# Kernel tuning notes

Measured on AMD Instinct MI355X. Metric: run time of the kernel, lower is better.

## Reference

```python
import jax, jax.numpy as jnp
import numpy as np

EPS = 1e-06

def setup_inputs() -> dict:
    key = jax.random.key(0)
    kx, kq, kk, kv = jax.random.split(key, 4)
    B, S, D, F = 8, 4096, 1024, 1024
    # glorot-uniform-ish scale for weights
    scale = (6.0 / (D + F)) ** 0.5
    x = jax.random.normal(kx, (B, S, D), dtype=jnp.float32)
    Wq = jax.random.uniform(kq, (D, F), dtype=jnp.float32, minval=-scale, maxval=scale)
    Wk = jax.random.uniform(kk, (D, F), dtype=jnp.float32, minval=-scale, maxval=scale)
    Wv = jax.random.uniform(kv, (D, F), dtype=jnp.float32, minval=-scale, maxval=scale)
    return {"x": x, "Wq": Wq, "Wk": Wk, "Wv": Wv}


def reference(x, Wq, Wk, Wv):
    # x: [B, S, D]; projections -> [B, S, F]
    queries = jnp.einsum('bsd,df->bsf', x, Wq)
    keys = jnp.einsum('bsd,df->bsf', x, Wk)
    values = jnp.einsum('bsd,df->bsf', x, Wv)
    # feature map: relu(.) + 1 (strictly positive kernel features)
    queries = jax.nn.relu(queries) + 1.0
    keys = jax.nn.relu(keys) + 1.0
    # numerator: K^T V over sequence -> [B, F, F]
    numerator = jnp.einsum('bsf,bsg->bfg', keys, values)
    # denominator: sum of keys over sequence -> [B, 1, F]; broadcasts over last axis
    denominator = jnp.sum(keys, axis=-2, keepdims=True)
    context = numerator / (denominator + EPS)
    # output: context @ Q^T -> [B, F, S]
    output = jnp.einsum('bfg,bsg->bfs', context, queries)
    return output
```

## Files before the change

### kernel.cpp

```cpp
#include <hip/hip_runtime.h>


#define EPSF 1e-6f

constexpr int Bb = 8;
constexpr int Ss = 4096;
constexpr int Dd = 1024;
constexpr int Ff = 1024;

typedef __attribute__((ext_vector_type(8))) short   bf16x8;
typedef __attribute__((ext_vector_type(8))) unsigned short u16x8;
typedef __attribute__((ext_vector_type(4))) float   f32x4;

typedef __attribute__((address_space(3))) unsigned char lds_u8;
typedef __attribute__((address_space(3))) const bf16x8  lds_cvec;

static __device__ __forceinline__ unsigned short f2bf(float f) {
    union { float f; unsigned int u; } v; v.f = f;
    unsigned int r = (v.u + 0x7fffu + ((v.u >> 16) & 1u)) >> 16;
    return (unsigned short)r;
}
static __device__ __forceinline__ float bf2f(unsigned short u) {
    union { unsigned int u; float f; } v; v.u = ((unsigned int)u) << 16;
    return v.f;
}

static __device__ __forceinline__ void gld_lds16(const void* g, lds_u8* l) {
    __builtin_amdgcn_global_load_lds(
        (const __attribute__((address_space(1))) unsigned int*)g,
        (__attribute__((address_space(3))) unsigned int*)l,
        16, 0, 0);
}

__global__ void cvt_x_kernel(const float* __restrict__ x, unsigned short* __restrict__ xb, int n4)
{
    int i = blockIdx.x * blockDim.x + threadIdx.x;
    if (i >= n4) return;
    float4 v = *(const float4*)&x[(size_t)i * 4];
    ushort4 o;
    o.x = f2bf(v.x); o.y = f2bf(v.y); o.z = f2bf(v.z); o.w = f2bf(v.w);
    *(ushort4*)&xb[(size_t)i * 4] = o;
}

__global__ void cvt_wT_kernel(const float* __restrict__ Wq,
                              const float* __restrict__ Wk,
                              const float* __restrict__ Wv,
                              unsigned short* __restrict__ WT)
{
    const int z = blockIdx.z;
    const float* __restrict__ W = (z == 0) ? Wq : (z == 1 ? Wk : Wv);
    unsigned short* __restrict__ dst = WT + (size_t)z * Dd * Ff;

    __shared__ float tile[32][33];
    const int tid = threadIdx.x;
    const int d0 = blockIdx.y * 32, f0 = blockIdx.x * 32;
    const int c = tid & 31, r8 = tid >> 5;
#pragma unroll
    for (int p = 0; p < 4; ++p) {
        int r = p * 8 + r8;
        tile[r][c] = W[(size_t)(d0 + r) * Ff + f0 + c];
    }
    __syncthreads();
#pragma unroll
    for (int p = 0; p < 4; ++p) {
        int r = p * 8 + r8;
        dst[(size_t)(f0 + r) * Dd + d0 + c] = f2bf(tile[c][r]);
    }
}

__global__ void add_ctx_kernel(const unsigned short* __restrict__ p,
                               unsigned short* __restrict__ c)
{
    const int b = blockIdx.y;
    const size_t i8 = ((size_t)blockIdx.x * 256 + threadIdx.x) * 8;
    const u16x8 a0 = *(const u16x8*)(p + (size_t)(2 * b) * Ff * Ff + i8);
    const u16x8 a1 = *(const u16x8*)(p + (size_t)(2 * b + 1) * Ff * Ff + i8);
    u16x8 o;
#pragma unroll
    for (int j = 0; j < 8; ++j) o[j] = f2bf(bf2f(a0[j]) + bf2f(a1[j]));
    *(u16x8*)(c + (size_t)b * Ff * Ff + i8) = o;
}

template<int ACT, int SCALE, int OUT_BF16, int SPLITK2, int DENACC, int KVSEL>
__global__ __launch_bounds__(512, 2)
void gemm8(const unsigned short* __restrict__ A,
           const unsigned short* __restrict__ Bt,
           void* __restrict__ Cout,
           const float* __restrict__ den,
           float* __restrict__ denw,
           int lda, int ldb, int ldc, int Kdim,
           size_t strideA, size_t strideB, size_t strideC)
{
    __shared__ __align__(16) unsigned char smem_[131072];
    lds_u8* const smem = (lds_u8*)smem_;

    const int gx = gridDim.x, gxy = gx * gridDim.y;
    int flat = blockIdx.z * gxy + blockIdx.y * gx + blockIdx.x;
    const int nwg = gxy * gridDim.z;
    const int cpx = nwg >> 3;
    flat = (flat & 7) * cpx + (flat >> 3);
    const int z = flat / gxy;
    const int rem = flat - z * gxy;
    const int by = rem / gx;
    const int bx = rem - by * gx;

    const int pid  = KVSEL ? (z & 1) : 0;
    const int zb   = KVSEL ? (z >> 1) : (SPLITK2 ? (z >> 1) : z);
    const int koff = SPLITK2 ? ((z & 1) * Kdim) : 0;
    const size_t cslab = KVSEL ? (size_t)(pid * Bb + zb) : (size_t)z;

    const unsigned short* __restrict__ Ag  =
        A + strideA * zb + koff + (KVSEL ? (size_t)pid * Dd * Ff : 0);
    const unsigned short* __restrict__ Bg  = Bt + strideB * zb + koff;
    const float* __restrict__ denb = SCALE ? (den + (size_t)zb * Ff) : nullptr;

    const int bm = by * 256;
    const int bn = bx * 256;

    const int tid  = threadIdx.x;
    const int wv   = tid >> 6, lane = tid & 63;
    const int wm   = wv >> 2, wn = wv & 3;
    const int lm   = lane & 15;
    const int kg16 = (lane >> 4) << 4;
    const int swz  = (lm & 7) << 4;
    const int kbs  = (((tid & 7) ^ ((tid >> 3) & 7)) << 4);
    const int srow = tid >> 3;

    f32x4 acc[8][4];
#pragma unroll
    for (int i = 0; i < 8; ++i)
#pragma unroll
        for (int j = 0; j < 4; ++j) acc[i][j] = (f32x4){0.f, 0.f, 0.f, 0.f};

    lds_u8* const A0 = smem;
    lds_u8* const B0 = smem + 32768;
    lds_u8* const A1 = smem + 65536;
    lds_u8* const B1 = smem + 98304;

    auto STAGE = [&](int ts, int m, int buf, int h) {
        const unsigned short* gb = m ? Bg : Ag;
        const int ld = m ? ldb : lda;
        const int off0 = m ? bn : bm;
        lds_u8* lb = smem + buf * 65536 + m * 32768 + h * 16384 + wv * 1024;
#pragma unroll
        for (int q = 0; q < 2; ++q) {
            int row = h * 128 + q * 64 + srow;
            const unsigned char* g =
                (const unsigned char*)(gb + (size_t)(off0 + row) * ld + ts * 64) + kbs;
            gld_lds16(g, lb + q * 8192);
        }
    };
    auto LDA4 = [&](bf16x8* dst, int fmb, int kk, lds_u8* Ab) {
#pragma unroll
        for (int f = 0; f < 4; ++f) {
            int r = wm * 128 + (fmb + f) * 16 + lm;
            dst[f] = *(lds_cvec*)(Ab + r * 128 + ((kk * 64 + kg16) ^ swz));
        }
    };
    auto LDB4 = [&](bf16x8* dst, int kk, lds_u8* Bb) {
#pragma unroll
        for (int f = 0; f < 4; ++f) {
            int c = wn * 64 + f * 16 + lm;
            dst[f] = *(lds_cvec*)(Bb + c * 128 + ((kk * 64 + kg16) ^ swz));
        }
    };

#define MM16(a4, b4, mo)                                                        \
    do {                                                                        \
        __builtin_amdgcn_s_setprio(1);                                          \
        _Pragma("unroll")                                                       \
        for (int fm = 0; fm < 4; ++fm)                                          \
            _Pragma("unroll")                                                   \
            for (int fn = 0; fn < 4; ++fn)                                      \
                acc[(mo) + fm][fn] = __builtin_amdgcn_mfma_f32_16x16x32_bf16(   \
                    (b4)[fn], (a4)[fm], acc[(mo) + fm][fn], 0, 0, 0);           \
        __builtin_amdgcn_s_setprio(0);                                          \
    } while (0)

#define PHEND()                                                     \
    do {                                                            \
        asm volatile("s_waitcnt lgkmcnt(0)");                       \
        __builtin_amdgcn_sched_barrier(0);                          \
        __builtin_amdgcn_s_barrier();                               \
    } while (0)
#define PHEND_VM2()                                                 \
    do {                                                            \
        asm volatile("s_waitcnt vmcnt(2) lgkmcnt(0)");              \
        __builtin_amdgcn_sched_barrier(0);                          \
        __builtin_amdgcn_s_barrier();                               \
    } while (0)

    const int NT = Kdim >> 6;
    const int NI = NT >> 1;

    STAGE(0, 1, 0, 0); STAGE(0, 1, 0, 1);
    STAGE(0, 0, 0, 0); STAGE(0, 0, 0, 1);
    STAGE(1, 1, 1, 0); STAGE(1, 1, 1, 1);
    asm volatile("s_waitcnt vmcnt(4)");
    __builtin_amdgcn_s_barrier();

    bf16x8 a03[4], a47[4], b0[4], b1[4];
    LDB4(b0, 0, B0); LDA4(a03, 0, 0, A0);

    for (int i = 0; i < NI; ++i) {
        const int t = 2 * i;
        const int t1s = t + 1;
        const int t2s = (t + 2 < NT) ? t + 2 : NT - 1;
        const int t3s = (t + 3 < NT) ? t + 3 : NT - 1;

        STAGE(t1s, 0, 1, 0);
        LDA4(a47, 4, 0, A0);
        MM16(a03, b0, 0);
        PHEND();
        STAGE(t1s, 0, 1, 1);
        LDA4(a03, 0, 1, A0); LDB4(b1, 1, B0);
        MM16(a47, b0, 4);
        PHEND();
        STAGE(t2s, 1, 0, 0);
        LDA4(a47, 4, 1, A0);
        MM16(a03, b1, 0);
        PHEND_VM2();
        STAGE(t2s, 1, 0, 1);
        LDA4(a03, 0, 0, A1); LDB4(b0, 0, B1);
        MM16(a47, b1, 4);
        PHEND();
        STAGE(t2s, 0, 0, 0);
        LDA4(a47, 4, 0, A1);
        MM16(a03, b0, 0);
        PHEND();
        STAGE(t2s, 0, 0, 1);
        LDA4(a03, 0, 1, A1); LDB4(b1, 1, B1);
        MM16(a47, b0, 4);
        PHEND();
        STAGE(t3s, 1, 1, 0);
        LDA4(a47, 4, 1, A1);
        MM16(a03, b1, 0);
        PHEND_VM2();
        STAGE(t3s, 1, 1, 1);
        LDA4(a03, 0, 0, A0); LDB4(b0, 0, B0);
        MM16(a47, b1, 4);
        PHEND();
    }

    asm volatile("s_waitcnt vmcnt(0)");

    const bool actv = ACT || (KVSEL && pid == 0);
    const bool dacc = DENACC || (KVSEL && pid == 0);
    const int hi4 = (lane >> 4) * 4;
#pragma unroll
    for (int fm = 0; fm < 8; ++fm) {
        const int gr = bm + wm * 128 + fm * 16 + lm;
        float rowsum = 0.f;
#pragma unroll
        for (int fn = 0; fn < 4; ++fn) {
            const int gcn = bn + wn * 64 + fn * 16 + hi4;
            f32x4 v = acc[fm][fn];
            if (actv) {
#pragma unroll
                for (int e = 0; e < 4; ++e) v[e] = fmaxf(v[e], 0.f) + 1.f;
            }
            if (dacc) rowsum += v[0] + v[1] + v[2] + v[3];
            if (SCALE) {
                float4 d4 = *(const float4*)&denb[gcn];
                v[0] *= 1.f / (d4.x + EPSF);
                v[1] *= 1.f / (d4.y + EPSF);
                v[2] *= 1.f / (d4.z + EPSF);
                v[3] *= 1.f / (d4.w + EPSF);
            }
            if (OUT_BF16) {
                ushort4 o;
                o.x = f2bf(v[0]); o.y = f2bf(v[1]); o.z = f2bf(v[2]); o.w = f2bf(v[3]);
                *(ushort4*)((unsigned short*)Cout + strideC * cslab + (size_t)gr * ldc + gcn) = o;
            } else {
                *(float4*)((float*)Cout + strideC * cslab + (size_t)gr * ldc + gcn) =
                    *(float4*)&v;
            }
        }
        if (dacc) {
            rowsum += __shfl_xor(rowsum, 16, 64);
            rowsum += __shfl_xor(rowsum, 32, 64);
            if (lane < 16) atomicAdd(denw + (size_t)zb * Ff + gr, rowsum);
        }
    }
#undef MM16
#undef PHEND
#undef PHEND_VM2
}

extern "C" void kernel_launch(void* const* d_in, const int* in_sizes, int n_in,
                              void* d_out, int out_size, void* d_ws, size_t ws_size,
                              hipStream_t stream)
{
    (void)in_sizes; (void)n_in; (void)out_size;
    const float* x  = (const float*)d_in[0];
    const float* Wq = (const float*)d_in[1];
    const float* Wk = (const float*)d_in[2];
    const float* Wv = (const float*)d_in[3];
    float* out = (float*)d_out;

    const size_t nx   = (size_t)Bb * Ss * Dd;
    const size_t nW   = (size_t)3 * Dd * Ff;
    const size_t nQKV = (size_t)Bb * Ss * Ff;
    const size_t nCtx = (size_t)Bb * Ff * Ff;
    const size_t nP   = (size_t)16 * Ff * Ff;

    unsigned short* xb   = (unsigned short*)d_ws;
    unsigned short* WT   = xb + nx;
    unsigned short* Qb   = WT + nW;
    unsigned short* KbT  = Qb + nQKV;
    unsigned short* VbT  = KbT + nQKV;
    unsigned short* ctxb = VbT + nQKV;
    float* den = (float*)(ctxb + nCtx);
    unsigned short* pctx = (unsigned short*)(den + (size_t)Bb * Ff);

    const size_t need_split =
        ((nx + nW + 3 * nQKV + nCtx + nP) * 2 + (size_t)Bb * Ff * 4);
    const bool do_split = ws_size >= need_split;

    cvt_x_kernel<<<dim3((int)(nx / 4 / 256)), 256, 0, stream>>>(x, xb, (int)(nx / 4));
    cvt_wT_kernel<<<dim3(Ff / 32, Dd / 32, 3), 256, 0, stream>>>(Wq, Wk, Wv, WT);

    hipMemsetAsync(den, 0, (size_t)Bb * Ff * sizeof(float), stream);

    gemm8<0, 0, 1, 0, 0, 1><<<dim3(Ss / 256, Ff / 256, 2 * Bb), 512, 0, stream>>>(
        WT + (size_t)1 * Dd * Ff, xb, KbT, nullptr, den,
        Dd, Dd, Ss, Dd, 0, (size_t)Ss * Dd, (size_t)Ff * Ss);

    gemm8<1, 1, 1, 0, 0, 0><<<dim3(Ff / 256, Ss / 256, Bb), 512, 0, stream>>>(
        xb, WT + (size_t)0 * Dd * Ff, Qb, den, nullptr,
        Dd, Dd, Ff, Dd, (size_t)Ss * Dd, 0, (size_t)Ss * Ff);

    if (do_split) {
        gemm8<0, 0, 1, 1, 0, 0><<<dim3(Ff / 256, Ff / 256, 2 * Bb), 512, 0, stream>>>(
            KbT, VbT, pctx, nullptr, nullptr,
            Ss, Ss, Ff, Ss / 2, (size_t)Ff * Ss, (size_t)Ff * Ss, (size_t)Ff * Ff);
        add_ctx_kernel<<<dim3(Ff * Ff / 8 / 256, Bb), 256, 0, stream>>>(pctx, ctxb);
    } else {
        gemm8<0, 0, 1, 0, 0, 0><<<dim3(Ff / 256, Ff / 256, Bb), 512, 0, stream>>>(
            KbT, VbT, ctxb, nullptr, nullptr,
            Ss, Ss, Ff, Ss, (size_t)Ff * Ss, (size_t)Ff * Ss, (size_t)Ff * Ff);
    }

    gemm8<0, 0, 0, 0, 0, 0><<<dim3(Ss / 256, Ff / 256, Bb), 512, 0, stream>>>(
        ctxb, Qb, out, nullptr, nullptr,
        Ff, Ff, Ss, Ff, (size_t)Ff * Ff, (size_t)Ss * Ff, (size_t)Ff * Ss);
}
```

Baseline: 407.5 us.

## Fuse Q, K, V projections into one launch and move denominator scaling to context

The Q projection GEMM and the combined K/V projection GEMM are merged into a single launch with 3*B slabs, where the slab index picks the projection and its output layout. Before, Q had to wait for the K denominator, so it was scaled by 1/den inside its epilogue. That scaling now happens on the context matrix, in the split-K add kernel or in the non-split context GEMM epilogue, which removes the dependency between the two launches. The intent is fewer launches, a better-filled grid, and less tail imbalance. The risks are an uneven mix of tile orientations inside one grid and the extra den loads in the add kernel.

```diff
diff --git a/kernel.cpp b/kernel.cpp
--- a/kernel.cpp
+++ b/kernel.cpp
@@ -69,19 +69,25 @@
 }
 
 __global__ void add_ctx_kernel(const unsigned short* __restrict__ p,
-                               unsigned short* __restrict__ c)
+                               unsigned short* __restrict__ c,
+                               const float* __restrict__ den)
 {
     const int b = blockIdx.y;
     const size_t i8 = ((size_t)blockIdx.x * 256 + threadIdx.x) * 8;
+    const int g0 = (int)(i8 & (size_t)(Ff - 1));
     const u16x8 a0 = *(const u16x8*)(p + (size_t)(2 * b) * Ff * Ff + i8);
     const u16x8 a1 = *(const u16x8*)(p + (size_t)(2 * b + 1) * Ff * Ff + i8);
+    const float4 d0 = *(const float4*)&den[(size_t)b * Ff + g0];
+    const float4 d1 = *(const float4*)&den[(size_t)b * Ff + g0 + 4];
+    const float dv[8] = {d0.x, d0.y, d0.z, d0.w, d1.x, d1.y, d1.z, d1.w};
     u16x8 o;
 #pragma unroll
-    for (int j = 0; j < 8; ++j) o[j] = f2bf(bf2f(a0[j]) + bf2f(a1[j]));
+    for (int j = 0; j < 8; ++j)
+        o[j] = f2bf((bf2f(a0[j]) + bf2f(a1[j])) * (1.f / (dv[j] + EPSF)));
     *(u16x8*)(c + (size_t)b * Ff * Ff + i8) = o;
 }
 
-template<int ACT, int SCALE, int OUT_BF16, int SPLITK2, int DENACC, int KVSEL>
+template<int ACT, int SCALE, int OUT_BF16, int SPLITK2, int DENACC, int QKV>
 __global__ __launch_bounds__(512, 2)
 void gemm8(const unsigned short* __restrict__ A,
            const unsigned short* __restrict__ Bt,
@@ -104,18 +110,40 @@
     const int by = rem / gx;
     const int bx = rem - by * gx;
 
-    const int pid  = KVSEL ? (z & 1) : 0;
-    const int zb   = KVSEL ? (z >> 1) : (SPLITK2 ? (z >> 1) : z);
+    const int pid  = QKV ? (z % 3) : 0;
+    const int zb   = QKV ? (z / 3) : (SPLITK2 ? (z >> 1) : z);
     const int koff = SPLITK2 ? ((z & 1) * Kdim) : 0;
-    const size_t cslab = KVSEL ? (size_t)(pid * Bb + zb) : (size_t)z;
-
-    const unsigned short* __restrict__ Ag  =
-        A + strideA * zb + koff + (KVSEL ? (size_t)pid * Dd * Ff : 0);
-    const unsigned short* __restrict__ Bg  = Bt + strideB * zb + koff;
+
+    const unsigned short* __restrict__ Ag;
+    const unsigned short* __restrict__ Bg;
+    int bm, bn, ldcr;
+    size_t coff;
+    bool actv, dacc;
+    if (QKV) {
+        if (pid == 0) {
+            Ag = Bt + (size_t)zb * Ss * Dd;
+            Bg = A;
+            bm = bx * 256; bn = by * 256;
+            ldcr = Ff;
+            coff = (size_t)zb * Ss * Ff;
+            actv = true;  dacc = false;
+        } else {
+            Ag = A + (size_t)pid * Dd * Ff;
+            Bg = Bt + (size_t)zb * Ss * Dd;
+            bm = by * 256; bn = bx * 256;
+            ldcr = Ss;
+            coff = ((size_t)pid * Bb + zb) * ((size_t)Ff * Ss);
+            actv = (pid == 1); dacc = (pid == 1);
+        }
+    } else {
+        Ag = A + strideA * zb + koff;
+        Bg = Bt + strideB * zb + koff;
+        bm = by * 256; bn = bx * 256;
+        ldcr = ldc;
+        coff = strideC * (size_t)z;
+        actv = ACT; dacc = DENACC;
+    }
     const float* __restrict__ denb = SCALE ? (den + (size_t)zb * Ff) : nullptr;
-
-    const int bm = by * 256;
-    const int bn = bx * 256;
 
     const int tid  = threadIdx.x;
     const int wv   = tid >> 6, lane = tid & 63;
@@ -244,8 +272,6 @@
 
     asm volatile("s_waitcnt vmcnt(0)");
 
-    const bool actv = ACT || (KVSEL && pid == 0);
-    const bool dacc = DENACC || (KVSEL && pid == 0);
     const int hi4 = (lane >> 4) * 4;
 #pragma unroll
     for (int fm = 0; fm < 8; ++fm) {
@@ -270,9 +296,9 @@
             if (OUT_BF16) {
                 ushort4 o;
                 o.x = f2bf(v[0]); o.y = f2bf(v[1]); o.z = f2bf(v[2]); o.w = f2bf(v[3]);
-                *(ushort4*)((unsigned short*)Cout + strideC * cslab + (size_t)gr * ldc + gcn) = o;
+                *(ushort4*)((unsigned short*)Cout + coff + (size_t)gr * ldcr + gcn) = o;
             } else {
-                *(float4*)((float*)Cout + strideC * cslab + (size_t)gr * ldc + gcn) =
+                *(float4*)((float*)Cout + coff + (size_t)gr * ldcr + gcn) =
                     *(float4*)&v;
             }
         }
@@ -317,27 +343,23 @@
         ((nx + nW + 3 * nQKV + nCtx + nP) * 2 + (size_t)Bb * Ff * 4);
     const bool do_split = ws_size >= need_split;
 
+    hipMemsetAsync(den, 0, (size_t)Bb * Ff * sizeof(float), stream);
+
     cvt_x_kernel<<<dim3((int)(nx / 4 / 256)), 256, 0, stream>>>(x, xb, (int)(nx / 4));
     cvt_wT_kernel<<<dim3(Ff / 32, Dd / 32, 3), 256, 0, stream>>>(Wq, Wk, Wv, WT);
 
-    hipMemsetAsync(den, 0, (size_t)Bb * Ff * sizeof(float), stream);
-
-    gemm8<0, 0, 1, 0, 0, 1><<<dim3(Ss / 256, Ff / 256, 2 * Bb), 512, 0, stream>>>(
-        WT + (size_t)1 * Dd * Ff, xb, KbT, nullptr, den,
-        Dd, Dd, Ss, Dd, 0, (size_t)Ss * Dd, (size_t)Ff * Ss);
-
-    gemm8<1, 1, 1, 0, 0, 0><<<dim3(Ff / 256, Ss / 256, Bb), 512, 0, stream>>>(
-        xb, WT + (size_t)0 * Dd * Ff, Qb, den, nullptr,
-        Dd, Dd, Ff, Dd, (size_t)Ss * Dd, 0, (size_t)Ss * Ff);
+    gemm8<0, 0, 1, 0, 0, 1><<<dim3(Ss / 256, Ff / 256, 3 * Bb), 512, 0, stream>>>(
+        WT, xb, Qb, nullptr, den,
+        Dd, Dd, 0, Dd, 0, 0, 0);
 
     if (do_split) {
         gemm8<0, 0, 1, 1, 0, 0><<<dim3(Ff / 256, Ff / 256, 2 * Bb), 512, 0, stream>>>(
             KbT, VbT, pctx, nullptr, nullptr,
             Ss, Ss, Ff, Ss / 2, (size_t)Ff * Ss, (size_t)Ff * Ss, (size_t)Ff * Ff);
-        add_ctx_kernel<<<dim3(Ff * Ff / 8 / 256, Bb), 256, 0, stream>>>(pctx, ctxb);
+        add_ctx_kernel<<<dim3(Ff * Ff / 8 / 256, Bb), 256, 0, stream>>>(pctx, ctxb, den);
     } else {
-        gemm8<0, 0, 1, 0, 0, 0><<<dim3(Ff / 256, Ff / 256, Bb), 512, 0, stream>>>(
-            KbT, VbT, ctxb, nullptr, nullptr,
+        gemm8<0, 1, 1, 0, 0, 0><<<dim3(Ff / 256, Ff / 256, Bb), 512, 0, stream>>>(
+            KbT, VbT, ctxb, den, nullptr,
             Ss, Ss, Ff, Ss, (size_t)Ff * Ss, (size_t)Ff * Ss, (size_t)Ff * Ff);
     }
 
```

New measurement: 406.6 us. About the same (-0.2%).
